# Optimization experiments

Measured on AMD Instinct MI355X. Metric: run time of the kernel, lower is better.

Reference implementation:

```python
import jax, jax.numpy as jnp
import numpy as np

D = 768; H = 12; NL = 8; V = 128
LATENT = 1024; TA = 1000; L = 90; S = 1120; B = 8
PAD_IDX = 0


def sinu_pos(n, dim):
    # ScaledSinusoidalEmbedding basis (scale applied by caller)
    half = dim // 2
    inv_freq = 10000.0 ** (-(jnp.arange(half, dtype=jnp.float32) / half))
    ang = jnp.arange(n, dtype=jnp.float32)[:, None] * inv_freq[None, :]
    return jnp.concatenate([jnp.sin(ang), jnp.cos(ang)], axis=-1)  # [n, dim]


def ln(x, g):
    m = x.mean(-1, keepdims=True)
    v = ((x - m) ** 2).mean(-1, keepdims=True)
    return (x - m) * jax.lax.rsqrt(v + 1e-5) * g


def decoder(x, ln1_g, ln2_g, lnf_g, qkv_w, attn_o_w, fc_w, mlp_o_w):
    Bq, Sq, _ = x.shape
    dh = D // H
    causal = jnp.tril(jnp.ones((Sq, Sq), bool))
    for l in range(NL):
        h = ln(x, ln1_g[l])
        q, k, v = jnp.split(h @ qkv_w[l].T, 3, axis=-1)
        q = q.reshape(Bq, Sq, H, dh).transpose(0, 2, 1, 3)
        k = k.reshape(Bq, Sq, H, dh).transpose(0, 2, 1, 3)
        v = v.reshape(Bq, Sq, H, dh).transpose(0, 2, 1, 3)
        att = jnp.einsum('bhqd,bhkd->bhqk', q, k) / jnp.sqrt(jnp.asarray(dh, x.dtype))
        att = jax.nn.softmax(jnp.where(causal, att, -1e9), axis=-1)
        o = jnp.einsum('bhqk,bhkd->bhqd', att, v).transpose(0, 2, 1, 3).reshape(Bq, Sq, D)
        x = x + o @ attn_o_w[l].T
        h = ln(x, ln2_g[l])
        x = x + jax.nn.gelu(h @ fc_w[l].T, approximate=False) @ mlp_o_w[l].T
    return ln(x, lnf_g)


def setup_inputs() -> dict:
    key = jax.random.key(0)
    ks = iter(jax.random.split(key, 24))
    p = lambda shape: 0.02 * jax.random.normal(next(ks), shape, jnp.float32)
    inp = {}
    inp['audio'] = jax.random.normal(next(ks), (B, TA, LATENT), jnp.float32)
    inp['audio_lengths'] = jax.random.randint(next(ks), (B,), TA // 2, TA + 1)
    ll = jax.random.randint(next(ks), (B,), L // 2, L + 1)
    ll = ll.at[0].set(L)  # labels are padded to max label length in-batch
    inp['label_lengths'] = ll
    lab = jax.random.randint(next(ks), (B, L), 2, V)
    inp['labels'] = jnp.where(jnp.arange(L)[None, :] < ll[:, None], lab, PAD_IDX)
    inp['text_emb_w'] = p((V, D))
    inp['text_head_w'] = p((V, D))
    inp['audio_proj_w'] = p((D, LATENT))
    inp['audio_proj_b'] = jnp.zeros((D,), jnp.float32)
    inp['start_emb'] = p((D,))
    inp['audio_pos_scale'] = jnp.asarray(D ** -0.5, jnp.float32)
    inp['text_pos_scale'] = jnp.asarray(D ** -0.5, jnp.float32)
    inp['ln1_g'] = jnp.ones((NL, D), jnp.float32)
    inp['ln2_g'] = jnp.ones((NL, D), jnp.float32)
    inp['lnf_g'] = jnp.ones((D,), jnp.float32)
    inp['qkv_w'] = p((NL, 3 * D, D))
    inp['attn_o_w'] = p((NL, D, D))
    inp['fc_w'] = p((NL, 4 * D, D))
    inp['mlp_o_w'] = p((NL, D, 4 * D))
    return inp


def reference(audio, labels, audio_lengths, label_lengths, text_emb_w, text_head_w,
              audio_proj_w, audio_proj_b, start_emb, audio_pos_scale, text_pos_scale,
              ln1_g, ln2_g, lnf_g, qkv_w, attn_o_w, fc_w, mlp_o_w):
    # audio projection + scaled sinusoidal positions
    audio_h = audio @ audio_proj_w.T + audio_proj_b                  # [B,TA,D]
    audio_h = audio_h + sinu_pos(TA, D) * audio_pos_scale
    text_h = text_emb_w[labels] + sinu_pos(L, D) * text_pos_scale    # [B,L,D]

    # vectorized ragged packing: [audio[:al] | start_emb | text[:ll-1] | zero-pad] -> [B,S,D]
    pos = jnp.arange(S)[None, :]                                     # [1,S]
    al = audio_lengths[:, None]
    ll = label_lengths[:, None]
    aud = jnp.pad(audio_h, ((0, 0), (0, S - TA), (0, 0)))
    tj = jnp.clip(pos - al - 1, 0, L - 1)                            # text index per slot
    txt = jnp.take_along_axis(text_h, tj[:, :, None], axis=1)
    emb = jnp.where((pos < al)[..., None], aud,
          jnp.where((pos == al)[..., None], start_emb,
          jnp.where((pos < al + ll)[..., None], txt, 0.0)))

    x = decoder(emb, ln1_g, ln2_g, lnf_g, qkv_w, attn_o_w, fc_w, mlp_o_w)

    # gather text latents x[b, al:al+ll] padded to L (== labels.shape[1])
    j = jnp.arange(L)[None, :]
    gi = jnp.clip(al + j, 0, S - 1)
    lat = jnp.take_along_axis(x, gi[:, :, None], axis=1)             # [B,L,D]
    lat = jnp.where((j < ll)[..., None], lat, 0.0)
    logits = lat @ text_head_w.T                                     # [B,L,V]

    # cross entropy, ignore_index = PAD_IDX, mean over non-pad tokens
    logp = jax.nn.log_softmax(logits, axis=-1)
    nll = -jnp.take_along_axis(logp, labels[..., None], axis=-1)[..., 0]
    m = (labels != PAD_IDX).astype(jnp.float32)
    return jnp.sum(nll * m) / jnp.sum(m)
```

## Files before the change

kernel.cpp:

```cpp
#include <hip/hip_runtime.h>

#define D_   768
#define H_   12
#define NL_  8
#define V_   128
#define LAT_ 1024
#define TA_  1000
#define L_   90
#define S_   1120
#define B_   8
#define DH_  64
#define MROWS (B_*S_)

typedef __bf16 bf16x8_t __attribute__((ext_vector_type(8)));
typedef float  f32x4_t  __attribute__((ext_vector_type(4)));

__global__ void sniff_kernel(const void* __restrict__ ones_src,
                             int* __restrict__ flag, float* __restrict__ accum) {
  if (threadIdx.x == 0) {
    unsigned w = *(const unsigned*)ones_src;
    flag[0] = (w == 0x3F803F80u) ? 1 : 0;
    accum[0] = 0.0f;
    accum[1] = 0.0f;
  }
}

__global__ __launch_bounds__(256) void cvt_kernel(const void* __restrict__ src,
    long off, __bf16* __restrict__ dst, int n, const int* __restrict__ flag) {
  long i = (long)blockIdx.x * 256 + threadIdx.x;
  const long stride = (long)gridDim.x * 256;
  if (*flag) {
    const __bf16* s = (const __bf16*)src + off;
    for (; i < n; i += stride) dst[i] = s[i];
  } else {
    const float* s = (const float*)src + off;
    for (; i < n; i += stride) dst[i] = (__bf16)s[i];
  }
}

template<int EPI>
__global__ __launch_bounds__(256) void gemm_kernel(
    const __bf16* __restrict__ A, const __bf16* __restrict__ W,
    void* __restrict__ Cout, const __bf16* __restrict__ bias,
    int M, int N, int K)
{
  __shared__ __align__(16) __bf16 As[128*32];
  __shared__ __align__(16) __bf16 Ws[128*32];
  const int tid  = threadIdx.x;
  const int wave = tid >> 6, lane = tid & 63;
  const int wm = wave >> 1, wn = wave & 1;
  const int lrow = lane & 15, lquad = lane >> 4;
  const int bm = blockIdx.y * 128, bn = blockIdx.x * 128;

  f32x4_t acc[4][4] = {};

  for (int kk = 0; kk < K; kk += 32) {
    #pragma unroll
    for (int p = 0; p < 2; ++p) {
      int c   = tid + p*256;
      int row = c >> 2;
      int kc  = (c & 3) * 8;
      int ga  = bm + row; ga = ga < M ? ga : (M-1);
      *reinterpret_cast<bf16x8_t*>(&As[row*32 + kc]) =
          *reinterpret_cast<const bf16x8_t*>(&A[(size_t)ga*K + kk + kc]);
      *reinterpret_cast<bf16x8_t*>(&Ws[row*32 + kc]) =
          *reinterpret_cast<const bf16x8_t*>(&W[(size_t)(bn+row)*K + kk + kc]);
    }
    __syncthreads();
    bf16x8_t af[4], bfr[4];
    #pragma unroll
    for (int i = 0; i < 4; ++i)
      af[i] = *reinterpret_cast<const bf16x8_t*>(&As[(wm*64 + i*16 + lrow)*32 + lquad*8]);
    #pragma unroll
    for (int j = 0; j < 4; ++j)
      bfr[j] = *reinterpret_cast<const bf16x8_t*>(&Ws[(wn*64 + j*16 + lrow)*32 + lquad*8]);
    #pragma unroll
    for (int i = 0; i < 4; ++i)
      #pragma unroll
      for (int j = 0; j < 4; ++j)
        acc[i][j] = __builtin_amdgcn_mfma_f32_16x16x32_bf16(af[i], bfr[j], acc[i][j], 0, 0, 0);
    __syncthreads();
  }

  const int orow0 = bm + wm*64 + lquad*4;
  const int ocol0 = bn + wn*64 + lrow;
  #pragma unroll
  for (int i = 0; i < 4; ++i) {
    #pragma unroll
    for (int j = 0; j < 4; ++j) {
      #pragma unroll
      for (int r = 0; r < 4; ++r) {
        int row = orow0 + i*16 + r;
        int col = ocol0 + j*16;
        if (row < M) {
          float v = acc[i][j][r];
          if (EPI == 0) {
            ((__bf16*)Cout)[(size_t)row*N + col] = (__bf16)v;
          } else if (EPI == 1) {
            ((float*)Cout)[(size_t)row*N + col] = v + (float)bias[col];
          } else if (EPI == 2) {
            ((float*)Cout)[(size_t)row*N + col] += v;
          } else {
            float gv = 0.5f * v * (1.0f + erff(v * 0.70710678118654752f));
            ((__bf16*)Cout)[(size_t)row*N + col] = (__bf16)gv;
          }
        }
      }
    }
  }
}

template<bool F32OUT>
__global__ __launch_bounds__(256) void ln_kernel(const float* __restrict__ x,
    const __bf16* __restrict__ g, void* __restrict__ outp)
{
  const int row = blockIdx.x;
  const int tid = threadIdx.x;
  const float* xr = x + (size_t)row * D_;
  float v0 = xr[tid], v1 = xr[tid+256], v2 = xr[tid+512];
  float s  = v0+v1+v2;
  float sq = v0*v0 + v1*v1 + v2*v2;
  #pragma unroll
  for (int off = 32; off > 0; off >>= 1) {
    s  += __shfl_down(s,  off);
    sq += __shfl_down(sq, off);
  }
  __shared__ float ps[4], pq[4];
  __shared__ float smean, srstd;
  const int wave = tid >> 6, lane = tid & 63;
  if (lane == 0) { ps[wave] = s; pq[wave] = sq; }
  __syncthreads();
  if (tid == 0) {
    float S4 = ps[0]+ps[1]+ps[2]+ps[3];
    float Q4 = pq[0]+pq[1]+pq[2]+pq[3];
    float mean = S4 * (1.0f/D_);
    float var  = Q4 * (1.0f/D_) - mean*mean;
    smean = mean;
    srstd = rsqrtf(var + 1e-5f);
  }
  __syncthreads();
  const float mean = smean, rstd = srstd;
  if (F32OUT) {
    float* o = (float*)outp + (size_t)row*D_;
    o[tid]     = (v0-mean)*rstd*(float)g[tid];
    o[tid+256] = (v1-mean)*rstd*(float)g[tid+256];
    o[tid+512] = (v2-mean)*rstd*(float)g[tid+512];
  } else {
    __bf16* o = (__bf16*)outp + (size_t)row*D_;
    o[tid]     = (__bf16)((v0-mean)*rstd*(float)g[tid]);
    o[tid+256] = (__bf16)((v1-mean)*rstd*(float)g[tid+256]);
    o[tid+512] = (__bf16)((v2-mean)*rstd*(float)g[tid+512]);
  }
}

__device__ __forceinline__ float sinu_pe(int pindex, int d) {
  int d2 = (d < 384) ? d : d - 384;
  float invf = __expf(-((float)d2 / 384.0f) * 9.210340371976184f);
  float ang  = (float)pindex * invf;
  return (d < 384) ? sinf(ang) : cosf(ang);
}

__global__ __launch_bounds__(256) void embed_kernel(const float* __restrict__ audio_h,
    const int* __restrict__ labels, const int* __restrict__ alen, const int* __restrict__ llen,
    const __bf16* __restrict__ temb, const __bf16* __restrict__ semb,
    const __bf16* __restrict__ aps, const __bf16* __restrict__ tps,
    float* __restrict__ x)
{
  const int bp = blockIdx.x;
  const int b = bp / S_, pos = bp % S_;
  const int a = alen[b], t = llen[b];
  float* xr = x + (size_t)bp * D_;
  if (pos < a) {
    const float apsf = (float)aps[0];
    const float* ar = audio_h + ((size_t)b*TA_ + pos)*D_;
    for (int d = threadIdx.x; d < D_; d += 256)
      xr[d] = ar[d] + sinu_pe(pos, d) * apsf;
  } else if (pos == a) {
    for (int d = threadIdx.x; d < D_; d += 256) xr[d] = (float)semb[d];
  } else if (pos < a + t) {
    const float tpsf = (float)tps[0];
    int tj = pos - a - 1;
    tj = tj < 0 ? 0 : (tj > L_-1 ? L_-1 : tj);
    int tok = labels[b*L_ + tj];
    const __bf16* tr = temb + (size_t)tok * D_;
    for (int d = threadIdx.x; d < D_; d += 256)
      xr[d] = (float)tr[d] + sinu_pe(tj, d) * tpsf;
  } else {
    for (int d = threadIdx.x; d < D_; d += 256) xr[d] = 0.0f;
  }
}

#define KSTR 72
#define VSTR 40
#define PSTR 40

__global__ __launch_bounds__(256) void attn_kernel(const __bf16* __restrict__ qkv,
                                                   __bf16* __restrict__ outp)
{
  __shared__ __align__(16) __bf16 Ks[32*KSTR];
  __shared__ __align__(16) __bf16 Vt[64*VSTR];
  __shared__ __align__(16) __bf16 Ps[4][32*PSTR];
  const int tid  = threadIdx.x;
  const int wave = tid >> 6, lane = tid & 63;
  const int lrow = lane & 15, lquad = lane >> 4;
  const int bh = blockIdx.y;
  const int b = bh / H_, h = bh % H_;
  const int q0 = ((int)gridDim.x - 1 - (int)blockIdx.x) * 128;

  bf16x8_t qf[2][2];
  #pragma unroll
  for (int i = 0; i < 2; ++i) {
    int q = q0 + wave*32 + i*16 + lrow;
    int qc2 = q < S_ ? q : S_-1;
    const __bf16* qp = qkv + ((size_t)(b*S_ + qc2))*(3*D_) + h*DH_;
    #pragma unroll
    for (int kc = 0; kc < 2; ++kc)
      qf[i][kc] = *reinterpret_cast<const bf16x8_t*>(qp + kc*32 + lquad*8);
  }

  f32x4_t o[2][4] = {};
  float m_i[2][4], l_i[2][4];
  #pragma unroll
  for (int i = 0; i < 2; ++i)
    #pragma unroll
    for (int r = 0; r < 4; ++r) { m_i[i][r] = -1e30f; l_i[i][r] = 0.0f; }

  const int kend = min(q0 + 127, S_-1);
  for (int kt = 0; kt <= kend; kt += 32) {
    {
      int j = tid >> 3, d0 = (tid & 7)*8;
      const __bf16* kp = qkv + ((size_t)(b*S_ + kt + j))*(3*D_) + D_ + h*DH_ + d0;
      *reinterpret_cast<bf16x8_t*>(&Ks[j*KSTR + d0]) =
          *reinterpret_cast<const bf16x8_t*>(kp);
      int d = tid & 63, kb = tid >> 6;
      const __bf16* vp = qkv + ((size_t)(b*S_ + kt + kb*8))*(3*D_) + 2*D_ + h*DH_ + d;
      bf16x8_t v8;
      #pragma unroll
      for (int e = 0; e < 8; ++e) v8[e] = vp[(size_t)e*(3*D_)];
      *reinterpret_cast<bf16x8_t*>(&Vt[d*VSTR + kb*8]) = v8;
    }
    __syncthreads();

    bf16x8_t kf[2][2];
    #pragma unroll
    for (int j2 = 0; j2 < 2; ++j2)
      #pragma unroll
      for (int kc = 0; kc < 2; ++kc)
        kf[j2][kc] = *reinterpret_cast<const bf16x8_t*>(
            &Ks[(j2*16 + lrow)*KSTR + kc*32 + lquad*8]);
    f32x4_t s[2][2] = {};
    #pragma unroll
    for (int i = 0; i < 2; ++i)
      #pragma unroll
      for (int j2 = 0; j2 < 2; ++j2) {
        s[i][j2] = __builtin_amdgcn_mfma_f32_16x16x32_bf16(qf[i][0], kf[j2][0], s[i][j2], 0,0,0);
        s[i][j2] = __builtin_amdgcn_mfma_f32_16x16x32_bf16(qf[i][1], kf[j2][1], s[i][j2], 0,0,0);
      }

    #pragma unroll
    for (int i = 0; i < 2; ++i) {
      #pragma unroll
      for (int r = 0; r < 4; ++r) {
        const int qrow = q0 + wave*32 + i*16 + lquad*4 + r;
        float mx = -1e30f;
        #pragma unroll
        for (int j2 = 0; j2 < 2; ++j2) {
          int key = kt + j2*16 + lrow;
          float sv = s[i][j2][r] * 0.125f;
          sv = (key <= qrow) ? sv : -1e30f;
          s[i][j2][r] = sv;
          mx = fmaxf(mx, sv);
        }
        mx = fmaxf(mx, __shfl_xor(mx, 1));
        mx = fmaxf(mx, __shfl_xor(mx, 2));
        mx = fmaxf(mx, __shfl_xor(mx, 4));
        mx = fmaxf(mx, __shfl_xor(mx, 8));
        const float mnew  = fmaxf(m_i[i][r], mx);
        const float alpha = __expf(m_i[i][r] - mnew);
        float psum = 0.0f;
        #pragma unroll
        for (int j2 = 0; j2 < 2; ++j2) {
          float pv = __expf(s[i][j2][r] - mnew);
          s[i][j2][r] = pv;
          psum += pv;
        }
        psum += __shfl_xor(psum, 1);
        psum += __shfl_xor(psum, 2);
        psum += __shfl_xor(psum, 4);
        psum += __shfl_xor(psum, 8);
        l_i[i][r] = l_i[i][r]*alpha + psum;
        m_i[i][r] = mnew;
        #pragma unroll
        for (int n = 0; n < 4; ++n) o[i][n][r] *= alpha;
      }
    }

    __bf16* pw = &Ps[wave][0];
    #pragma unroll
    for (int i = 0; i < 2; ++i)
      #pragma unroll
      for (int j2 = 0; j2 < 2; ++j2)
        #pragma unroll
        for (int r = 0; r < 4; ++r)
          pw[(i*16 + lquad*4 + r)*PSTR + j2*16 + lrow] = (__bf16)s[i][j2][r];
    bf16x8_t pf[2];
    #pragma unroll
    for (int i = 0; i < 2; ++i)
      pf[i] = *reinterpret_cast<const bf16x8_t*>(&pw[(i*16 + lrow)*PSTR + lquad*8]);
    bf16x8_t vf[4];
    #pragma unroll
    for (int n = 0; n < 4; ++n)
      vf[n] = *reinterpret_cast<const bf16x8_t*>(&Vt[(n*16 + lrow)*VSTR + lquad*8]);
    #pragma unroll
    for (int i = 0; i < 2; ++i)
      #pragma unroll
      for (int n = 0; n < 4; ++n)
        o[i][n] = __builtin_amdgcn_mfma_f32_16x16x32_bf16(pf[i], vf[n], o[i][n], 0,0,0);
    __syncthreads();
  }

  #pragma unroll
  for (int i = 0; i < 2; ++i) {
    const int qb = q0 + wave*32 + i*16 + lquad*4;
    #pragma unroll
    for (int r = 0; r < 4; ++r) {
      if (qb + r < S_) {
        float inv = 1.0f / l_i[i][r];
        __bf16* orow = outp + ((size_t)(b*S_ + qb + r))*D_ + h*DH_ + lrow;
        #pragma unroll
        for (int n = 0; n < 4; ++n)
          orow[n*16] = (__bf16)(o[i][n][r] * inv);
      }
    }
  }
}

__global__ __launch_bounds__(128) void head_loss_kernel(const float* __restrict__ xf,
    const int* __restrict__ labels, const int* __restrict__ alen,
    const int* __restrict__ llen, const __bf16* __restrict__ hw,
    float* __restrict__ accum)
{
  const int bj = blockIdx.x;
  const int b = bj / L_, j = bj % L_;
  const int lab = labels[b*L_ + j];
  if (lab == 0) return;
  int gi = alen[b] + j; gi = gi < S_-1 ? gi : S_-1;
  const float* row = xf + ((size_t)(b*S_ + gi))*D_;
  __shared__ float lr[D_];
  for (int d = threadIdx.x; d < D_; d += 128) lr[d] = row[d];
  __syncthreads();
  const int v = threadIdx.x;
  const __bf16* wrow = hw + (size_t)v*D_;
  float dot = 0.0f;
  for (int d = 0; d < D_; d += 8) {
    bf16x8_t w8 = *reinterpret_cast<const bf16x8_t*>(wrow + d);
    #pragma unroll
    for (int e = 0; e < 8; ++e) dot += lr[d+e]*(float)w8[e];
  }
  __shared__ float lg[V_];
  lg[v] = dot;
  __syncthreads();
  if (threadIdx.x == 0) {
    float mx = lg[0];
    for (int i = 1; i < V_; ++i) mx = fmaxf(mx, lg[i]);
    float se = 0.0f;
    for (int i = 0; i < V_; ++i) se += __expf(lg[i]-mx);
    float nll = (mx + logf(se)) - lg[lab];
    atomicAdd(accum, nll);
    atomicAdd(accum+1, 1.0f);
  }
}

__global__ void finalize_kernel(const float* __restrict__ accum,
                                const int* __restrict__ flag, void* __restrict__ out) {
  if (threadIdx.x == 0) {
    float v = accum[0] / accum[1];
    if (*flag) ((__bf16*)out)[0] = (__bf16)v;
    else       ((float*)out)[0]  = v;
  }
}

extern "C" void kernel_launch(void* const* d_in, const int* in_sizes, int n_in,
                              void* d_out, int out_size, void* d_ws, size_t ws_size,
                              hipStream_t stream)
{
  const void* audio        = d_in[0];
  const int*  audio_len    = (const int*)d_in[1];
  const int*  label_len    = (const int*)d_in[2];
  const int*  labels       = (const int*)d_in[3];
  const void* text_emb_w   = d_in[4];
  const void* text_head_w  = d_in[5];
  const void* audio_proj_w = d_in[6];
  const void* audio_proj_b = d_in[7];
  const void* start_emb    = d_in[8];
  const void* aps          = d_in[9];
  const void* tps          = d_in[10];
  const void* ln1_g        = d_in[11];
  const void* ln2_g        = d_in[12];
  const void* lnf_g        = d_in[13];
  const void* qkv_w        = d_in[14];
  const void* attn_o_w     = d_in[15];
  const void* fc_w         = d_in[16];
  const void* mlp_o_w      = d_in[17];

  char* p = (char*)d_ws;
  auto alloc = [&](size_t bytes) {
    char* r = p;
    p += (bytes + 255) & ~(size_t)255;
    return r;
  };
  int*    flag    = (int*)   alloc(64);
  float*  accum   = (float*) alloc(192);
  float*  x       = (float*) alloc((size_t)MROWS*D_*4);
  __bf16* hbuf    = (__bf16*)alloc((size_t)MROWS*D_*2);
  __bf16* qkvbuf  = (__bf16*)alloc((size_t)MROWS*3*D_*2);
  __bf16* attnout = (__bf16*)alloc((size_t)MROWS*D_*2);
  __bf16* ffnbuf  = (__bf16*)alloc((size_t)MROWS*4*D_*2);
  __bf16* wbuf    = (__bf16*)alloc((size_t)4*D_*D_*2);
  __bf16* temb_b  = (__bf16*)alloc((size_t)V_*D_*2);
  __bf16* thead_b = (__bf16*)alloc((size_t)V_*D_*2);
  __bf16* apw_b   = (__bf16*)alloc((size_t)D_*LAT_*2);
  __bf16* apb_b   = (__bf16*)alloc((size_t)D_*2);
  __bf16* semb_b  = (__bf16*)alloc((size_t)D_*2);
  __bf16* aps_b   = (__bf16*)alloc(64);
  __bf16* tps_b   = (__bf16*)alloc(64);
  __bf16* ln1_b   = (__bf16*)alloc((size_t)NL_*D_*2);
  __bf16* ln2_b   = (__bf16*)alloc((size_t)NL_*D_*2);
  __bf16* lnf_b   = (__bf16*)alloc((size_t)D_*2);
  __bf16* audio_bf = qkvbuf;
  float*  audio_h  = (float*)ffnbuf;
  float*  xf       = (float*)ffnbuf;

  auto cvt = [&](const void* src, long off, __bf16* dst, long n) {
    int blocks = (int)(((n + 255) / 256) < 512 ? ((n + 255) / 256) : 512);
    cvt_kernel<<<blocks, 256, 0, stream>>>(src, off, dst, (int)n, flag);
  };

  sniff_kernel<<<1, 64, 0, stream>>>(lnf_g, flag, accum);

  cvt(audio,        0, audio_bf, (long)B_*TA_*LAT_);
  cvt(text_emb_w,   0, temb_b,   (long)V_*D_);
  cvt(text_head_w,  0, thead_b,  (long)V_*D_);
  cvt(audio_proj_w, 0, apw_b,    (long)D_*LAT_);
  cvt(audio_proj_b, 0, apb_b,    D_);
  cvt(start_emb,    0, semb_b,   D_);
  cvt(aps,          0, aps_b,    1);
  cvt(tps,          0, tps_b,    1);
  cvt(ln1_g,        0, ln1_b,    (long)NL_*D_);
  cvt(ln2_g,        0, ln2_b,    (long)NL_*D_);
  cvt(lnf_g,        0, lnf_b,    D_);

  gemm_kernel<1><<<dim3(D_/128, (B_*TA_ + 127)/128), 256, 0, stream>>>(
      audio_bf, apw_b, audio_h, apb_b, B_*TA_, D_, LAT_);
  embed_kernel<<<MROWS, 256, 0, stream>>>(audio_h, labels, audio_len, label_len,
      temb_b, semb_b, aps_b, tps_b, x);

  for (int l = 0; l < NL_; ++l) {
    ln_kernel<false><<<MROWS, 256, 0, stream>>>(x, ln1_b + l*D_, hbuf);
    cvt(qkv_w, (long)l*3*D_*D_, wbuf, (long)3*D_*D_);
    gemm_kernel<0><<<dim3(3*D_/128, MROWS/128), 256, 0, stream>>>(
        hbuf, wbuf, qkvbuf, nullptr, MROWS, 3*D_, D_);
    attn_kernel<<<dim3((S_ + 127)/128, B_*H_), 256, 0, stream>>>(qkvbuf, attnout);
    cvt(attn_o_w, (long)l*D_*D_, wbuf, (long)D_*D_);
    gemm_kernel<2><<<dim3(D_/128, MROWS/128), 256, 0, stream>>>(
        attnout, wbuf, x, nullptr, MROWS, D_, D_);
    ln_kernel<false><<<MROWS, 256, 0, stream>>>(x, ln2_b + l*D_, hbuf);
    cvt(fc_w, (long)l*4*D_*D_, wbuf, (long)4*D_*D_);
    gemm_kernel<3><<<dim3(4*D_/128, MROWS/128), 256, 0, stream>>>(
        hbuf, wbuf, ffnbuf, nullptr, MROWS, 4*D_, D_);
    cvt(mlp_o_w, (long)l*4*D_*D_, wbuf, (long)4*D_*D_);
    gemm_kernel<2><<<dim3(D_/128, MROWS/128), 256, 0, stream>>>(
        ffnbuf, wbuf, x, nullptr, MROWS, D_, 4*D_);
  }

  ln_kernel<true><<<MROWS, 256, 0, stream>>>(x, lnf_b, xf);
  head_loss_kernel<<<B_*L_, 128, 0, stream>>>(xf, labels, audio_len, label_len,
                                              thead_b, accum);
  finalize_kernel<<<1, 64, 0, stream>>>(accum, flag, d_out);
}
```

Measured before the change: 3.845 ms.

## Use direct global-to-LDS loads in GEMM and vectorize dtype conversion

The GEMM tile loads now go straight from global memory into LDS through the global_load_lds builtin. This skips the round trip through registers and precomputes the per-thread addresses outside the k-loop. The input conversion kernel now handles 8 elements per thread with vector loads and stores, which should cut the cost of converting the large audio tensor. The LDS layout relies on the builtin's lane-contiguous write pattern matching the 16-row-by-32 tile, and there is no explicit wait beyond __syncthreads. Sizes not divisible by 8 that are larger than 8 would silently drop their tail elements.

New measurement: 3.704 ms. 3.7% less time.

```diff
diff --git a/kernel.cpp b/kernel.cpp
--- a/kernel.cpp
+++ b/kernel.cpp
@@ -25,17 +25,40 @@
   }
 }
 
-__global__ __launch_bounds__(256) void cvt_kernel(const void* __restrict__ src,
-    long off, __bf16* __restrict__ dst, int n, const int* __restrict__ flag) {
+__global__ __launch_bounds__(256) void cvt8_kernel(const void* __restrict__ src,
+    long off, __bf16* __restrict__ dst, long n8, const int* __restrict__ flag) {
   long i = (long)blockIdx.x * 256 + threadIdx.x;
   const long stride = (long)gridDim.x * 256;
   if (*flag) {
-    const __bf16* s = (const __bf16*)src + off;
-    for (; i < n; i += stride) dst[i] = s[i];
+    const bf16x8_t* s = (const bf16x8_t*)((const __bf16*)src + off);
+    bf16x8_t* d = (bf16x8_t*)dst;
+    for (; i < n8; i += stride) d[i] = s[i];
   } else {
     const float* s = (const float*)src + off;
-    for (; i < n; i += stride) dst[i] = (__bf16)s[i];
-  }
+    for (; i < n8; i += stride) {
+      float4 a = *(const float4*)(s + i*8);
+      float4 b = *(const float4*)(s + i*8 + 4);
+      bf16x8_t v;
+      v[0]=(__bf16)a.x; v[1]=(__bf16)a.y; v[2]=(__bf16)a.z; v[3]=(__bf16)a.w;
+      v[4]=(__bf16)b.x; v[5]=(__bf16)b.y; v[6]=(__bf16)b.z; v[7]=(__bf16)b.w;
+      *(bf16x8_t*)(dst + i*8) = v;
+    }
+  }
+}
+
+__global__ void cvt1_kernel(const void* __restrict__ src, long off,
+    __bf16* __restrict__ dst, int n, const int* __restrict__ flag) {
+  int i = threadIdx.x;
+  if (i < n) {
+    if (*flag) dst[i] = ((const __bf16*)src + off)[i];
+    else       dst[i] = (__bf16)((const float*)src + off)[i];
+  }
+}
+
+__device__ __forceinline__ void gload_lds16(const __bf16* g, __bf16* l) {
+  __builtin_amdgcn_global_load_lds(
+      (const __attribute__((address_space(1))) void*)g,
+      (__attribute__((address_space(3))) void*)l, 16, 0, 0);
 }
 
 template<int EPI>
@@ -52,21 +75,29 @@
   const int lrow = lane & 15, lquad = lane >> 4;
   const int bm = blockIdx.y * 128, bn = blockIdx.x * 128;
 
+  const int c0    = wave*2;
+  const int srow0 = c0*16 + (lane >> 2);
+  const int kc8   = (lane & 3) * 8;
+  const int gaA0  = min(bm + srow0,      M-1);
+  const int gaA1  = min(bm + srow0 + 16, M-1);
+  const size_t a0 = (size_t)gaA0*K + kc8;
+  const size_t a1 = (size_t)gaA1*K + kc8;
+  const size_t w0 = (size_t)(bn + srow0)*K + kc8;
+  const size_t w1 = (size_t)(bn + srow0 + 16)*K + kc8;
+  __bf16* ldsA0 = &As[ c0   *512 + lane*8];
+  __bf16* ldsA1 = &As[(c0+1)*512 + lane*8];
+  __bf16* ldsW0 = &Ws[ c0   *512 + lane*8];
+  __bf16* ldsW1 = &Ws[(c0+1)*512 + lane*8];
+
   f32x4_t acc[4][4] = {};
 
   for (int kk = 0; kk < K; kk += 32) {
-    #pragma unroll
-    for (int p = 0; p < 2; ++p) {
-      int c   = tid + p*256;
-      int row = c >> 2;
-      int kc  = (c & 3) * 8;
-      int ga  = bm + row; ga = ga < M ? ga : (M-1);
-      *reinterpret_cast<bf16x8_t*>(&As[row*32 + kc]) =
-          *reinterpret_cast<const bf16x8_t*>(&A[(size_t)ga*K + kk + kc]);
-      *reinterpret_cast<bf16x8_t*>(&Ws[row*32 + kc]) =
-          *reinterpret_cast<const bf16x8_t*>(&W[(size_t)(bn+row)*K + kk + kc]);
-    }
+    gload_lds16(&A[a0 + kk], ldsA0);
+    gload_lds16(&A[a1 + kk], ldsA1);
+    gload_lds16(&W[w0 + kk], ldsW0);
+    gload_lds16(&W[w1 + kk], ldsW1);
     __syncthreads();
+
     bf16x8_t af[4], bfr[4];
     #pragma unroll
     for (int i = 0; i < 4; ++i)
@@ -432,8 +463,13 @@
   float*  xf       = (float*)ffnbuf;
 
   auto cvt = [&](const void* src, long off, __bf16* dst, long n) {
-    int blocks = (int)(((n + 255) / 256) < 512 ? ((n + 255) / 256) : 512);
-    cvt_kernel<<<blocks, 256, 0, stream>>>(src, off, dst, (int)n, flag);
+    if (n >= 8) {
+      long n8 = n >> 3;
+      int blocks = (int)((n8 + 255) / 256 < 512 ? (n8 + 255) / 256 : 512);
+      cvt8_kernel<<<blocks, 256, 0, stream>>>(src, off, dst, n8, flag);
+    } else {
+      cvt1_kernel<<<1, 64, 0, stream>>>(src, off, dst, (int)n, flag);
+    }
   };
 
   sniff_kernel<<<1, 64, 0, stream>>>(lnf_g, flag, accum);
```
